# Kernel tuning notes

Measured on AMD Instinct MI355X. Metric: run time of the kernel, lower is better.

## Reference

```python
import jax, jax.numpy as jnp
import numpy as np

IN_C, DIM, OUT_C, N_PIECES = 3, 256, 256, 20
BATCH, SET_N = 16, 128


def _xavier(k, shape, fan_in, fan_out):
    limit = float(np.sqrt(6.0 / (fan_in + fan_out)))
    return jax.random.uniform(k, shape, jnp.float32, -limit, limit)


def setup_inputs() -> dict:
    key = jax.random.key(0)
    ks = jax.random.split(key, 9)
    return {
        "x": jax.random.normal(ks[0], (BATCH, IN_C, SET_N), jnp.float32),
        "conv1_w": _xavier(ks[1], (DIM, IN_C), IN_C, DIM),
        "conv1_b": jnp.zeros((DIM,), jnp.float32),
        "conv2_w": _xavier(ks[2], (DIM, DIM), DIM, DIM),
        "conv2_b": jnp.zeros((DIM,), jnp.float32),
        "pool_w": jax.random.normal(ks[3], (DIM, N_PIECES + 1), jnp.float32) * 0.1,
        "lin1_w": _xavier(ks[4], (DIM, DIM), DIM, DIM),
        "lin1_b": jnp.zeros((DIM,), jnp.float32),
        "lin2_w": _xavier(ks[5], (OUT_C, DIM), DIM, OUT_C),
        "lin2_b": jnp.zeros((OUT_C,), jnp.float32),
        "cls1_w": _xavier(ks[6], (OUT_C, OUT_C), OUT_C, OUT_C),
        "cls1_b": jnp.zeros((OUT_C,), jnp.float32),
        "cls2_w": _xavier(ks[7], (10, OUT_C), OUT_C, 10),
        "cls2_b": jnp.zeros((10,), jnp.float32),
    }


def _fspool(x, pool_w, tau=1.0):
    # x: (B, C, N); pool_w: (C, N_PIECES+1). n is None -> full sets, mask is all ones.
    B, C, N = x.shape
    # piecewise-linear continuous weights evaluated at ratios i/(N-1)
    ratios = jnp.clip(jnp.arange(N, dtype=x.dtype) / max(N - 1, 1), 0.0, 1.0)  # (N,)
    idx_f = N_PIECES * ratios
    idx = jnp.floor(idx_f).astype(jnp.int32)
    frac = idx_f - idx.astype(x.dtype)
    left = pool_w[:, idx]                                   # (C, N)
    right = pool_w[:, jnp.clip(idx + 1, 0, N_PIECES)]       # (C, N)
    w = (1.0 - frac) * left + frac * right                  # (C, N)
    # relaxed continuous sort (NeuralSort / deterministic_sort), descending
    s = x.reshape(B * C, N, 1)
    A = jnp.abs(s - jnp.swapaxes(s, 1, 2))                  # (BC, N, N)
    Bsum = A.sum(axis=2, keepdims=True)                     # == A @ 1 1^T rowsums, (BC, N, 1)
    scaling = (N + 1 - 2 * (jnp.arange(N) + 1)).astype(x.dtype)  # (N,)
    Cmat = s * scaling[None, None, :]                       # (BC, N, N)
    P = jax.nn.softmax(jnp.swapaxes(Cmat - Bsum, 1, 2) / tau, axis=-1)  # (BC, N, N)
    xs = jnp.matmul(P, s).reshape(B, C, N)                  # soft-sorted, descending
    pooled = (xs * w[None]).sum(axis=2)                     # (B, C)
    return pooled, P


def reference(x, conv1_w, conv1_b, conv2_w, conv2_b, pool_w,
              lin1_w, lin1_b, lin2_w, lin2_b, cls1_w, cls1_b, cls2_w, cls2_b):
    # conv1x1 stack: (B, IN_C, N) -> (B, DIM, N)
    h = jnp.einsum('dc,bcn->bdn', conv1_w, x) + conv1_b[None, :, None]
    h = jax.nn.relu(h)
    h = jnp.einsum('dc,bcn->bdn', conv2_w, h) + conv2_b[None, :, None]
    pooled, _ = _fspool(h, pool_w)                          # (B, DIM)
    z = jax.nn.relu(pooled @ lin1_w.T + lin1_b)
    z = z @ lin2_w.T + lin2_b                               # (B, OUT_C)
    z = jax.nn.relu(z @ cls1_w.T + cls1_b)
    return z @ cls2_w.T + cls2_b                            # (B, 10)
```

## Files before the change

kernel.cpp:

```cpp
#include <hip/hip_runtime.h>
#include <math.h>


#if __has_builtin(__builtin_amdgcn_exp2f)
#define EXP2F(x) __builtin_amdgcn_exp2f(x)
#else
#define EXP2F(x) exp2f(x)
#endif

__device__ __forceinline__ float pool_weight(const float* __restrict__ pw, int j)
{
    float ratio = (float)j / 127.0f;
    float idx_f = 20.0f * ratio;
    int idx = (int)idx_f;
    float frac = idx_f - (float)idx;
    int idx2 = idx + 1 > 20 ? 20 : idx + 1;
    return (1.0f - frac) * pw[idx] + frac * pw[idx2];
}

__global__ __launch_bounds__(256) void conv_pool_kernel(
    const float* __restrict__ x,   const float* __restrict__ w1,
    const float* __restrict__ b1,  const float* __restrict__ W2,
    const float* __restrict__ b2,  const float* __restrict__ pool_w,
    float* __restrict__ pooled)
{
    const float LOG2E = 1.4426950408889634f;
    __shared__ float4 xa4[128];
    __shared__ float4 w1p[256];
    __shared__ float  Ast[4][32];
    __shared__ float2 Bsp[32][65];
    __shared__ float2 sbp[4][128];

    int tid = threadIdx.x;
    int blk = blockIdx.x;
    int b   = blk >> 6;
    int c0  = (blk & 63) << 2;

    w1p[tid] = make_float4(w1[tid*3], w1[tid*3+1], w1[tid*3+2], b1[tid]);
    if (tid < 128)
        xa4[tid] = make_float4(x[b*384 + tid], x[b*384 + 128 + tid],
                               x[b*384 + 256 + tid], 0.0f);
    __syncthreads();

    int wid = tid >> 6, l = tid & 63;
    int krel = tid & 31, p0 = (tid >> 5) * 8;
    float acc0 = 0.f, acc1 = 0.f;

    for (int k0 = 0; k0 < 256; k0 += 32) {
        if (tid < 128)
            Ast[tid >> 5][tid & 31] =
                W2[(c0 + (tid >> 5)) * 256 + k0 + (tid & 31)];
        {
            float4 wv = w1p[k0 + krel];
            #pragma unroll
            for (int i = 0; i < 8; i++) {
                int p = p0 + i;
                float4 xlo = xa4[p];
                float4 xhi = xa4[p + 64];
                float h0 = fmaf(wv.x, xlo.x, fmaf(wv.y, xlo.y,
                           fmaf(wv.z, xlo.z, wv.w)));
                float h1 = fmaf(wv.x, xhi.x, fmaf(wv.y, xhi.y,
                           fmaf(wv.z, xhi.z, wv.w)));
                Bsp[krel][p] = make_float2(fmaxf(h0, 0.f), fmaxf(h1, 0.f));
            }
        }
        __syncthreads();
        float4 a4[8];
        #pragma unroll
        for (int q = 0; q < 8; q++)
            a4[q] = *(const float4*)&Ast[wid][q * 4];
        #pragma unroll
        for (int kk = 0; kk < 32; kk++) {
            float a = ((const float*)a4)[kk];
            float2 bv = Bsp[kk][l];
            acc0 = fmaf(a, bv.x, acc0);
            acc1 = fmaf(a, bv.y, acc1);
        }
        __syncthreads();
    }

    float bias = b2[c0 + wid];
    float s0 = acc0 + bias, s1 = acc1 + bias;
    sbp[wid][l]      = make_float2(s0, 0.f);
    sbp[wid][l + 64] = make_float2(s1, 0.f);

    float a0 = 0.f, a1 = 0.f, g0 = 0.f, g1 = 0.f;
    #pragma unroll 8
    for (int j = 0; j < 128; j += 2) {
        float4 p = *(const float4*)&sbp[wid][j];
        a0 += fabsf(s0 - p.x); a1 += fabsf(s0 - p.z);
        g0 += fabsf(s1 - p.x); g1 += fabsf(s1 - p.z);
    }
    sbp[wid][l].y      = (a0 + a1) * LOG2E;
    sbp[wid][l + 64].y = (g0 + g1) * LOG2E;

    float scal0 = (float)(127 - 2 * l) * LOG2E;
    float scal1 = (float)(-1 - 2 * l) * LOG2E;
    float m00 = -1e30f, m01 = -1e30f, m10 = -1e30f, m11 = -1e30f;
    #pragma unroll 8
    for (int i = 0; i < 128; i += 2) {
        float4 p = *(const float4*)&sbp[wid][i];
        m00 = fmaxf(m00, fmaf(p.x, scal0, -p.y));
        m01 = fmaxf(m01, fmaf(p.z, scal0, -p.w));
        m10 = fmaxf(m10, fmaf(p.x, scal1, -p.y));
        m11 = fmaxf(m11, fmaf(p.z, scal1, -p.w));
    }
    float m0 = fmaxf(m00, m01), m1 = fmaxf(m10, m11);

    float se0a = 0.f, se0b = 0.f, sd0a = 0.f, sd0b = 0.f;
    float se1a = 0.f, se1b = 0.f, sd1a = 0.f, sd1b = 0.f;
    #pragma unroll 4
    for (int i = 0; i < 128; i += 2) {
        float4 p = *(const float4*)&sbp[wid][i];
        float e0a = EXP2F(fmaf(p.x, scal0, -p.y) - m0);
        float e0b = EXP2F(fmaf(p.z, scal0, -p.w) - m0);
        float e1a = EXP2F(fmaf(p.x, scal1, -p.y) - m1);
        float e1b = EXP2F(fmaf(p.z, scal1, -p.w) - m1);
        se0a += e0a; sd0a = fmaf(e0a, p.x, sd0a);
        se0b += e0b; sd0b = fmaf(e0b, p.z, sd0b);
        se1a += e1a; sd1a = fmaf(e1a, p.x, sd1a);
        se1b += e1b; sd1b = fmaf(e1b, p.z, sd1b);
    }
    float xs0 = (sd0a + sd0b) / (se0a + se0b);
    float xs1 = (sd1a + sd1b) / (se1a + se1b);

    int c = c0 + wid;
    const float* pw = pool_w + c * 21;
    float part = xs0 * pool_weight(pw, l) + xs1 * pool_weight(pw, l + 64);
    #pragma unroll
    for (int off = 32; off > 0; off >>= 1)
        part += __shfl_xor(part, off);
    if (l == 0) pooled[b * 256 + c] = part;
}

__global__ __launch_bounds__(256) void tail_kernel(
    const float* __restrict__ pooled,
    const float* __restrict__ L1w, const float* __restrict__ L1b,
    const float* __restrict__ L2w, const float* __restrict__ L2b,
    const float* __restrict__ C1w, const float* __restrict__ C1b,
    const float* __restrict__ C2w, const float* __restrict__ C2b,
    float* __restrict__ out)
{
    __shared__ float za[256], zb[256];
    int bt = blockIdx.x, tid = threadIdx.x;
    za[tid] = pooled[bt * 256 + tid];
    __syncthreads();
    {
        float acc = L1b[tid];
        const float* wr = L1w + tid * 256;
        #pragma unroll 8
        for (int k = 0; k < 256; k += 4) {
            float4 wv = *(const float4*)(wr + k);
            float4 iv = *(const float4*)(&za[k]);
            acc = fmaf(wv.x, iv.x, acc); acc = fmaf(wv.y, iv.y, acc);
            acc = fmaf(wv.z, iv.z, acc); acc = fmaf(wv.w, iv.w, acc);
        }
        zb[tid] = fmaxf(acc, 0.f);
    }
    __syncthreads();
    {
        float acc = L2b[tid];
        const float* wr = L2w + tid * 256;
        #pragma unroll 8
        for (int k = 0; k < 256; k += 4) {
            float4 wv = *(const float4*)(wr + k);
            float4 iv = *(const float4*)(&zb[k]);
            acc = fmaf(wv.x, iv.x, acc); acc = fmaf(wv.y, iv.y, acc);
            acc = fmaf(wv.z, iv.z, acc); acc = fmaf(wv.w, iv.w, acc);
        }
        za[tid] = acc;
    }
    __syncthreads();
    {
        float acc = C1b[tid];
        const float* wr = C1w + tid * 256;
        #pragma unroll 8
        for (int k = 0; k < 256; k += 4) {
            float4 wv = *(const float4*)(wr + k);
            float4 iv = *(const float4*)(&za[k]);
            acc = fmaf(wv.x, iv.x, acc); acc = fmaf(wv.y, iv.y, acc);
            acc = fmaf(wv.z, iv.z, acc); acc = fmaf(wv.w, iv.w, acc);
        }
        zb[tid] = fmaxf(acc, 0.f);
    }
    __syncthreads();
    if (tid < 160) {
        int o = tid >> 4, kk = tid & 15;
        const float* wr = C2w + o * 256;
        float pp = 0.f;
        #pragma unroll
        for (int k = kk * 16; k < kk * 16 + 16; k++)
            pp = fmaf(zb[k], wr[k], pp);
        pp += __shfl_down(pp, 8, 16);
        pp += __shfl_down(pp, 4, 16);
        pp += __shfl_down(pp, 2, 16);
        pp += __shfl_down(pp, 1, 16);
        if (kk == 0) out[bt * 10 + o] = pp + C2b[o];
    }
}

extern "C" void kernel_launch(void* const* d_in, const int* in_sizes, int n_in,
                              void* d_out, int out_size, void* d_ws, size_t ws_size,
                              hipStream_t stream)
{
    (void)in_sizes; (void)n_in; (void)out_size; (void)ws_size;
    const float* x       = (const float*)d_in[0];
    const float* conv1_w = (const float*)d_in[1];
    const float* conv1_b = (const float*)d_in[2];
    const float* conv2_w = (const float*)d_in[3];
    const float* conv2_b = (const float*)d_in[4];
    const float* pool_w  = (const float*)d_in[5];
    const float* lin1_w  = (const float*)d_in[6];
    const float* lin1_b  = (const float*)d_in[7];
    const float* lin2_w  = (const float*)d_in[8];
    const float* lin2_b  = (const float*)d_in[9];
    const float* cls1_w  = (const float*)d_in[10];
    const float* cls1_b  = (const float*)d_in[11];
    const float* cls2_w  = (const float*)d_in[12];
    const float* cls2_b  = (const float*)d_in[13];
    float* out = (float*)d_out;

    float* pooled = (float*)d_ws;

    conv_pool_kernel<<<1024, 256, 0, stream>>>(
        x, conv1_w, conv1_b, conv2_w, conv2_b, pool_w, pooled);
    tail_kernel<<<16, 256, 0, stream>>>(pooled,
        lin1_w, lin1_b, lin2_w, lin2_b, cls1_w, cls1_b, cls2_w, cls2_b, out);
}
```

Baseline: 64.69 us.

## Use online softmax, register-resident conv1 inputs, and 512-thread tail MLP

Conv1 inputs are now held in per-thread registers instead of LDS, and the layer-1 activations are written to the B tile as float4 stores. The two-pass softmax (max pass, then exp-sum pass) becomes a single online pass that rescales running sums as the max changes. In exchange it evaluates twice as many exponentials. The tail MLP kernel moves to 512 threads, with two threads per output row combined by a shuffle, to shorten per-thread dot products. Together these aim to cut LDS traffic, the number of passes over the set, and the serial latency of the tail.

Measured after the change: 62.61 us. -3.2%, faster.

```diff
diff --git a/kernel.cpp b/kernel.cpp
--- a/kernel.cpp
+++ b/kernel.cpp
@@ -18,6 +18,17 @@
     return (1.0f - frac) * pw[idx] + frac * pw[idx2];
 }
 
+#define OSTEP(sv, bv, scal, m, se, sd)                      \
+    {                                                       \
+        float v_  = fmaf((sv), (scal), -(bv));              \
+        float mn_ = fmaxf((m), v_);                         \
+        float sc_ = EXP2F((m) - mn_);                       \
+        float e_  = EXP2F(v_ - mn_);                        \
+        (se) = fmaf((se), sc_, e_);                         \
+        (sd) = fmaf((sd), sc_, e_ * (sv));                  \
+        (m)  = mn_;                                         \
+    }
+
 __global__ __launch_bounds__(256) void conv_pool_kernel(
     const float* __restrict__ x,   const float* __restrict__ w1,
     const float* __restrict__ b1,  const float* __restrict__ W2,
@@ -25,44 +36,47 @@
     float* __restrict__ pooled)
 {
     const float LOG2E = 1.4426950408889634f;
-    __shared__ float4 xa4[128];
     __shared__ float4 w1p[256];
     __shared__ float  Ast[4][32];
-    __shared__ float2 Bsp[32][65];
-    __shared__ float2 sbp[4][128];
+    __shared__ float2 Bsp[32][66];
+    __shared__ float  ss[4][128];
+    __shared__ float  bb[4][128];
 
     int tid = threadIdx.x;
     int blk = blockIdx.x;
     int b   = blk >> 6;
     int c0  = (blk & 63) << 2;
 
+    int wid = tid >> 6, l = tid & 63;
+    int ng  = tid & 31;
+    int kg  = tid >> 5;
+    int n0  = ng * 2;
+
     w1p[tid] = make_float4(w1[tid*3], w1[tid*3+1], w1[tid*3+2], b1[tid]);
-    if (tid < 128)
-        xa4[tid] = make_float4(x[b*384 + tid], x[b*384 + 128 + tid],
-                               x[b*384 + 256 + tid], 0.0f);
-    __syncthreads();
-
-    int wid = tid >> 6, l = tid & 63;
-    int krel = tid & 31, p0 = (tid >> 5) * 8;
+    const float* xb = x + b * 384;
+    float x00 = xb[n0],          x01 = xb[n0 + 1];
+    float x0a = xb[n0 + 64],     x0b = xb[n0 + 65];
+    float x10 = xb[128 + n0],    x11 = xb[128 + n0 + 1];
+    float x1a = xb[128 + n0 + 64], x1b = xb[128 + n0 + 65];
+    float x20 = xb[256 + n0],    x21 = xb[256 + n0 + 1];
+    float x2a = xb[256 + n0 + 64], x2b = xb[256 + n0 + 65];
+    __syncthreads();
+
     float acc0 = 0.f, acc1 = 0.f;
 
     for (int k0 = 0; k0 < 256; k0 += 32) {
         if (tid < 128)
             Ast[tid >> 5][tid & 31] =
                 W2[(c0 + (tid >> 5)) * 256 + k0 + (tid & 31)];
-        {
+        #pragma unroll
+        for (int q = 0; q < 4; q++) {
+            int krel = kg * 4 + q;
             float4 wv = w1p[k0 + krel];
-            #pragma unroll
-            for (int i = 0; i < 8; i++) {
-                int p = p0 + i;
-                float4 xlo = xa4[p];
-                float4 xhi = xa4[p + 64];
-                float h0 = fmaf(wv.x, xlo.x, fmaf(wv.y, xlo.y,
-                           fmaf(wv.z, xlo.z, wv.w)));
-                float h1 = fmaf(wv.x, xhi.x, fmaf(wv.y, xhi.y,
-                           fmaf(wv.z, xhi.z, wv.w)));
-                Bsp[krel][p] = make_float2(fmaxf(h0, 0.f), fmaxf(h1, 0.f));
-            }
+            float h0 = fmaxf(fmaf(wv.x,x00, fmaf(wv.y,x10, fmaf(wv.z,x20, wv.w))), 0.f);
+            float h1 = fmaxf(fmaf(wv.x,x01, fmaf(wv.y,x11, fmaf(wv.z,x21, wv.w))), 0.f);
+            float ha = fmaxf(fmaf(wv.x,x0a, fmaf(wv.y,x1a, fmaf(wv.z,x2a, wv.w))), 0.f);
+            float hb = fmaxf(fmaf(wv.x,x0b, fmaf(wv.y,x1b, fmaf(wv.z,x2b, wv.w))), 0.f);
+            *(float4*)&Bsp[krel][n0] = make_float4(h0, ha, h1, hb);
         }
         __syncthreads();
         float4 a4[8];
@@ -81,48 +95,45 @@
 
     float bias = b2[c0 + wid];
     float s0 = acc0 + bias, s1 = acc1 + bias;
-    sbp[wid][l]      = make_float2(s0, 0.f);
-    sbp[wid][l + 64] = make_float2(s1, 0.f);
-
-    float a0 = 0.f, a1 = 0.f, g0 = 0.f, g1 = 0.f;
+    ss[wid][l]      = s0;
+    ss[wid][l + 64] = s1;
+
+    float a0=0,a1=0,a2=0,a3=0, g0=0,g1=0,g2=0,g3=0;
     #pragma unroll 8
-    for (int j = 0; j < 128; j += 2) {
-        float4 p = *(const float4*)&sbp[wid][j];
-        a0 += fabsf(s0 - p.x); a1 += fabsf(s0 - p.z);
-        g0 += fabsf(s1 - p.x); g1 += fabsf(s1 - p.z);
-    }
-    sbp[wid][l].y      = (a0 + a1) * LOG2E;
-    sbp[wid][l + 64].y = (g0 + g1) * LOG2E;
+    for (int j = 0; j < 128; j += 4) {
+        float4 s4 = *(const float4*)&ss[wid][j];
+        a0 += fabsf(s0 - s4.x); a1 += fabsf(s0 - s4.y);
+        a2 += fabsf(s0 - s4.z); a3 += fabsf(s0 - s4.w);
+        g0 += fabsf(s1 - s4.x); g1 += fabsf(s1 - s4.y);
+        g2 += fabsf(s1 - s4.z); g3 += fabsf(s1 - s4.w);
+    }
+    bb[wid][l]      = ((a0+a1)+(a2+a3)) * LOG2E;
+    bb[wid][l + 64] = ((g0+g1)+(g2+g3)) * LOG2E;
 
     float scal0 = (float)(127 - 2 * l) * LOG2E;
     float scal1 = (float)(-1 - 2 * l) * LOG2E;
-    float m00 = -1e30f, m01 = -1e30f, m10 = -1e30f, m11 = -1e30f;
-    #pragma unroll 8
-    for (int i = 0; i < 128; i += 2) {
-        float4 p = *(const float4*)&sbp[wid][i];
-        m00 = fmaxf(m00, fmaf(p.x, scal0, -p.y));
-        m01 = fmaxf(m01, fmaf(p.z, scal0, -p.w));
-        m10 = fmaxf(m10, fmaf(p.x, scal1, -p.y));
-        m11 = fmaxf(m11, fmaf(p.z, scal1, -p.w));
-    }
-    float m0 = fmaxf(m00, m01), m1 = fmaxf(m10, m11);
-
-    float se0a = 0.f, se0b = 0.f, sd0a = 0.f, sd0b = 0.f;
-    float se1a = 0.f, se1b = 0.f, sd1a = 0.f, sd1b = 0.f;
+    float mA0=-1e30f, mB0=-1e30f, mA1=-1e30f, mB1=-1e30f;
+    float seA0=0,seB0=0,sdA0=0,sdB0=0;
+    float seA1=0,seB1=0,sdA1=0,sdB1=0;
     #pragma unroll 4
-    for (int i = 0; i < 128; i += 2) {
-        float4 p = *(const float4*)&sbp[wid][i];
-        float e0a = EXP2F(fmaf(p.x, scal0, -p.y) - m0);
-        float e0b = EXP2F(fmaf(p.z, scal0, -p.w) - m0);
-        float e1a = EXP2F(fmaf(p.x, scal1, -p.y) - m1);
-        float e1b = EXP2F(fmaf(p.z, scal1, -p.w) - m1);
-        se0a += e0a; sd0a = fmaf(e0a, p.x, sd0a);
-        se0b += e0b; sd0b = fmaf(e0b, p.z, sd0b);
-        se1a += e1a; sd1a = fmaf(e1a, p.x, sd1a);
-        se1b += e1b; sd1b = fmaf(e1b, p.z, sd1b);
-    }
-    float xs0 = (sd0a + sd0b) / (se0a + se0b);
-    float xs1 = (sd1a + sd1b) / (se1a + se1b);
+    for (int i = 0; i < 128; i += 4) {
+        float4 s4 = *(const float4*)&ss[wid][i];
+        float4 b4 = *(const float4*)&bb[wid][i];
+        OSTEP(s4.x, b4.x, scal0, mA0, seA0, sdA0);
+        OSTEP(s4.y, b4.y, scal0, mB0, seB0, sdB0);
+        OSTEP(s4.z, b4.z, scal0, mA0, seA0, sdA0);
+        OSTEP(s4.w, b4.w, scal0, mB0, seB0, sdB0);
+        OSTEP(s4.x, b4.x, scal1, mA1, seA1, sdA1);
+        OSTEP(s4.y, b4.y, scal1, mB1, seB1, sdB1);
+        OSTEP(s4.z, b4.z, scal1, mA1, seA1, sdA1);
+        OSTEP(s4.w, b4.w, scal1, mB1, seB1, sdB1);
+    }
+    float m0  = fmaxf(mA0, mB0);
+    float scA = EXP2F(mA0 - m0), scB = EXP2F(mB0 - m0);
+    float xs0 = (sdA0 * scA + sdB0 * scB) / (seA0 * scA + seB0 * scB);
+    float m1  = fmaxf(mA1, mB1);
+    float tA  = EXP2F(mA1 - m1), tB = EXP2F(mB1 - m1);
+    float xs1 = (sdA1 * tA + sdB1 * tB) / (seA1 * tA + seB1 * tB);
 
     int c = c0 + wid;
     const float* pw = pool_w + c * 21;
@@ -133,7 +144,29 @@
     if (l == 0) pooled[b * 256 + c] = part;
 }
 
-__global__ __launch_bounds__(256) void tail_kernel(
+__device__ __forceinline__ void dense512(
+    const float* __restrict__ W, const float* __restrict__ Bv,
+    const float* in_lds, float* out_lds, int tid, bool do_relu)
+{
+    int o = tid >> 1, p = tid & 1;
+    const float* wr = W + o * 256 + p * 128;
+    const float* ir = in_lds + p * 128;
+    float acc = 0.f;
+    #pragma unroll
+    for (int k = 0; k < 128; k += 4) {
+        float4 wv = *(const float4*)(wr + k);
+        float4 iv = *(const float4*)(ir + k);
+        acc = fmaf(wv.x, iv.x, acc); acc = fmaf(wv.y, iv.y, acc);
+        acc = fmaf(wv.z, iv.z, acc); acc = fmaf(wv.w, iv.w, acc);
+    }
+    acc += __shfl_xor(acc, 1);
+    if (p == 0) {
+        acc += Bv[o];
+        out_lds[o] = do_relu ? fmaxf(acc, 0.f) : acc;
+    }
+}
+
+__global__ __launch_bounds__(512) void tail_kernel(
     const float* __restrict__ pooled,
     const float* __restrict__ L1w, const float* __restrict__ L1b,
     const float* __restrict__ L2w, const float* __restrict__ L2b,
@@ -143,59 +176,29 @@
 {
     __shared__ float za[256], zb[256];
     int bt = blockIdx.x, tid = threadIdx.x;
-    za[tid] = pooled[bt * 256 + tid];
-    __syncthreads();
-    {
-        float acc = L1b[tid];
-        const float* wr = L1w + tid * 256;
-        #pragma unroll 8
-        for (int k = 0; k < 256; k += 4) {
-            float4 wv = *(const float4*)(wr + k);
-            float4 iv = *(const float4*)(&za[k]);
-            acc = fmaf(wv.x, iv.x, acc); acc = fmaf(wv.y, iv.y, acc);
-            acc = fmaf(wv.z, iv.z, acc); acc = fmaf(wv.w, iv.w, acc);
-        }
-        zb[tid] = fmaxf(acc, 0.f);
-    }
-    __syncthreads();
-    {
-        float acc = L2b[tid];
-        const float* wr = L2w + tid * 256;
-        #pragma unroll 8
-        for (int k = 0; k < 256; k += 4) {
-            float4 wv = *(const float4*)(wr + k);
-            float4 iv = *(const float4*)(&zb[k]);
-            acc = fmaf(wv.x, iv.x, acc); acc = fmaf(wv.y, iv.y, acc);
-            acc = fmaf(wv.z, iv.z, acc); acc = fmaf(wv.w, iv.w, acc);
-        }
-        za[tid] = acc;
-    }
-    __syncthreads();
-    {
-        float acc = C1b[tid];
-        const float* wr = C1w + tid * 256;
-        #pragma unroll 8
-        for (int k = 0; k < 256; k += 4) {
-            float4 wv = *(const float4*)(wr + k);
-            float4 iv = *(const float4*)(&za[k]);
-            acc = fmaf(wv.x, iv.x, acc); acc = fmaf(wv.y, iv.y, acc);
-            acc = fmaf(wv.z, iv.z, acc); acc = fmaf(wv.w, iv.w, acc);
-        }
-        zb[tid] = fmaxf(acc, 0.f);
-    }
-    __syncthreads();
-    if (tid < 160) {
-        int o = tid >> 4, kk = tid & 15;
-        const float* wr = C2w + o * 256;
-        float pp = 0.f;
-        #pragma unroll
-        for (int k = kk * 16; k < kk * 16 + 16; k++)
-            pp = fmaf(zb[k], wr[k], pp);
-        pp += __shfl_down(pp, 8, 16);
-        pp += __shfl_down(pp, 4, 16);
-        pp += __shfl_down(pp, 2, 16);
-        pp += __shfl_down(pp, 1, 16);
-        if (kk == 0) out[bt * 10 + o] = pp + C2b[o];
+    if (tid < 256) za[tid] = pooled[bt * 256 + tid];
+    __syncthreads();
+    dense512(L1w, L1b, za, zb, tid, true);
+    __syncthreads();
+    dense512(L2w, L2b, zb, za, tid, false);
+    __syncthreads();
+    dense512(C1w, C1b, za, zb, tid, true);
+    __syncthreads();
+    if (tid < 320) {
+        int o = tid >> 5, kb = tid & 31;
+        const float* wr = C2w + o * 256 + kb * 8;
+        const float* ir = zb + kb * 8;
+        float4 w0 = *(const float4*)(wr);
+        float4 w1v = *(const float4*)(wr + 4);
+        float4 i0 = *(const float4*)(ir);
+        float4 i1 = *(const float4*)(ir + 4);
+        float p = fmaf(w0.x,i0.x, fmaf(w0.y,i0.y, fmaf(w0.z,i0.z,
+                  fmaf(w0.w,i0.w, fmaf(w1v.x,i1.x, fmaf(w1v.y,i1.y,
+                  fmaf(w1v.z,i1.z, w1v.w*i1.w)))))));
+        #pragma unroll
+        for (int off = 16; off > 0; off >>= 1)
+            p += __shfl_xor(p, off, 32);
+        if (kb == 0) out[bt * 10 + o] = p + C2b[o];
     }
 }
 
@@ -224,6 +227,6 @@
 
     conv_pool_kernel<<<1024, 256, 0, stream>>>(
         x, conv1_w, conv1_b, conv2_w, conv2_b, pool_w, pooled);
-    tail_kernel<<<16, 256, 0, stream>>>(pooled,
+    tail_kernel<<<16, 512, 0, stream>>>(pooled,
         lin1_w, lin1_b, lin2_w, lin2_b, cls1_w, cls1_b, cls2_w, cls2_b, out);
 }
```
